# Kernel optimization log

Hardware: AMD Instinct MI355X
Metric: run time of the kernel (lower is better)

Reference implementation:

```python
import jax, jax.numpy as jnp
import numpy as np
import math

NEG_INF = -10000.0

def setup_inputs() -> dict:
    key = jax.random.key(0)
    k1, k2, k3 = jax.random.split(key, 3)
    B, Sq, Sk, H, D = 2, 2048, 2048, 16, 64
    q = jax.random.normal(k1, (B, Sq, H, D), dtype=jnp.float32)
    kv = jax.random.normal(k2, (B, Sk, 2, H, D), dtype=jnp.float32)
    key_padding_mask = jax.random.randint(k3, (B, Sk), 0, 2).astype(jnp.bool_)
    return {"q": q, "kv": kv, "key_padding_mask": key_padding_mask}

def reference(q, kv, key_padding_mask):
    # q: (B, Sq, H, D); kv: (B, Sk, 2, H, D); key_padding_mask: (B, Sk) True=keep
    D = q.shape[-1]
    softmax_scale = 1.0 / math.sqrt(D)
    k = kv[:, :, 0]  # (B, Sk, H, D)
    v = kv[:, :, 1]  # (B, Sk, H, D)
    # (B, H, Sq, Sk) score matrix
    scores = jnp.einsum('bthd,bshd->bhts', q, k * softmax_scale)
    # additive padding mask: 0 where keep, NEG_INF where masked out
    pad = jnp.where(key_padding_mask, 0.0, NEG_INF).astype(scores.dtype)
    scores = scores + pad[:, None, None, :]
    attention = jax.nn.softmax(scores, axis=-1)
    # dropout_p = 0.0 (eval mode) -> no-op
    output = jnp.einsum('bhts,bshd->bthd', attention, v)
    return output
```

## Files before the change

### kernel.cpp

```cpp
#include <hip/hip_runtime.h>

typedef unsigned short u16;
typedef unsigned int   u32;
typedef u16   u16x8 __attribute__((ext_vector_type(8)));
typedef float f32x4 __attribute__((ext_vector_type(4)));
typedef float f32x16 __attribute__((ext_vector_type(16)));
typedef __bf16 bf16x8 __attribute__((ext_vector_type(8)));
typedef u32   u32x4 __attribute__((ext_vector_type(4)));

#define QSCALE  0.18033688011112f
#define BM_OPEN  -28.8539008177793f
#define BM_MASK  -14455.8043097f

__device__ __forceinline__ u16 f2bf(float x){
  __bf16 h = (__bf16)x;
  return __builtin_bit_cast(u16, h);
}
__device__ __forceinline__ f32x16 mfma32(u16x8 a, u16x8 b, f32x16 c){
  return __builtin_amdgcn_mfma_f32_32x32x16_bf16(
      __builtin_bit_cast(bf16x8, a), __builtin_bit_cast(bf16x8, b), c, 0, 0, 0);
}
__device__ __forceinline__ void gld16(const void* g, void* l){
  __builtin_amdgcn_global_load_lds(
      (const __attribute__((address_space(1))) u32*)g,
      (__attribute__((address_space(3))) u32*)l, 16, 0, 0);
}
__device__ __forceinline__ u32 cvtpk(float lo, float hi){
  u32 d;
  asm("v_cvt_pk_bf16_f32 %0, %1, %2" : "=v"(d) : "v"(lo), "v"(hi));
  return d;
}
__device__ __forceinline__ void plswap(u32 &x, u32 &y){
  asm("v_permlane32_swap_b32 %0, %1" : "+v"(x), "+v"(y));
}


__global__ __launch_bounds__(256, 4)
void prepass(const float* __restrict__ KV, const int* __restrict__ MASK,
             u16* __restrict__ IMG, float* __restrict__ BIASM)
{
  const int tid = threadIdx.x;
  const int bid = blockIdx.x;
  const int kt = bid & 31;
  const int h  = (bid >> 5) & 15;
  const int b  = bid >> 9;
  const int kb = kt*64;
  const size_t kv_b = (size_t)b*(2048u*2048u);
  u16* tile = IMG + (size_t)bid * 8192;

  {
    const int skey = tid >> 2, scp = tid & 3;
    const float* kp = KV + kv_b + (size_t)(kb + skey)*2048 + h*64 + 16*scp;
    f32x4 f0 = *(const f32x4*)(kp);
    f32x4 f1 = *(const f32x4*)(kp + 4);
    f32x4 f2 = *(const f32x4*)(kp + 8);
    f32x4 f3 = *(const f32x4*)(kp + 12);
    u16x8 c0, c1;
    #pragma unroll
    for (int e = 0; e < 4; ++e){
      c0[e] = f2bf(f0[e]); c0[e+4] = f2bf(f1[e]);
      c1[e] = f2bf(f2[e]); c1[e+4] = f2bf(f3[e]);
    }
    const int idx0 = skey*64 + (((2*scp) ^ (skey & 7)) << 3);
    *(u16x8*)&tile[idx0]     = c0;
    *(u16x8*)&tile[idx0 ^ 8] = c1;
  }
  {
    const int sdb = tid & 7, ssp = tid >> 3;
    const float* vp = KV + kv_b + (size_t)(kb + 2*ssp)*2048 + 1024 + h*64 + 8*sdb;
    f32x4 r0a = *(const f32x4*)(vp);
    f32x4 r0b = *(const f32x4*)(vp + 4);
    f32x4 r1a = *(const f32x4*)(vp + 2048);
    f32x4 r1b = *(const f32x4*)(vp + 2048 + 4);
    u32* vimg = (u32*)(tile + 4096);
    const int wc = ssp >> 2, wi = ssp & 3;
    #pragma unroll
    for (int j = 0; j < 4; ++j){
      const int d0 = 8*sdb + j;
      const int d1 = d0 + 4;
      vimg[d0*32 + ((wc ^ (d0 & 7)) << 2) + wi] = (u32)f2bf(r0a[j]) | ((u32)f2bf(r1a[j]) << 16);
      vimg[d1*32 + ((wc ^ (d1 & 7)) << 2) + wi] = (u32)f2bf(r0b[j]) | ((u32)f2bf(r1b[j]) << 16);
    }
  }
  if (h == 0 && tid < 64){
    const int s = kb + tid;
    BIASM[b*2048 + s] = MASK[b*2048 + s] ? BM_OPEN : BM_MASK;
  }
}

template<int PRE>
__global__ __launch_bounds__(256, 2)
void attn_main(const float* __restrict__ Q, const float* __restrict__ KV,
               const int* __restrict__ MASK, const u16* __restrict__ IMG,
               const float* __restrict__ BIASM, float* __restrict__ OUT)
{
  __shared__ __align__(16) u16 KVbuf[3][8192];
  __shared__ __align__(16) float BiasLds[2048];

  const int tid  = threadIdx.x;
  const int w    = tid >> 6;
  const int lane = tid & 63;
  const int hi   = lane >> 5;
  const int lq   = lane & 31;

  const int bid0 = blockIdx.x;
  const int bid  = (bid0 & 7)*64 + (bid0 >> 3);
  const int qt  = bid & 15;
  const int h   = (bid >> 4) & 15;
  const int b   = bid >> 8;

  const int qbase = qt*128 + w*32;
  const size_t q_b  = (size_t)b * (2048u*1024u);
  const size_t kv_b = (size_t)b * (2048u*2048u);

  const int sw7 = lq & 7;

  u16x8 Qf[4];
  {
    const int qrow = qbase + lq;
    const float* qp = Q + q_b + (size_t)qrow*1024 + h*64 + 8*hi;
    #pragma unroll
    for (int kc = 0; kc < 4; ++kc){
      f32x4 a = *(const f32x4*)(qp + 16*kc);
      f32x4 c = *(const f32x4*)(qp + 16*kc + 4);
      u16x8 v;
      #pragma unroll
      for (int e = 0; e < 4; ++e){
        v[e]     = f2bf(a[e] * QSCALE);
        v[e + 4] = f2bf(c[e] * QSCALE);
      }
      Qf[kc] = v;
    }
  }

  f32x16 Oa[2];
  #pragma unroll
  for (int dt = 0; dt < 2; ++dt)
    #pragma unroll
    for (int r = 0; r < 16; ++r) Oa[dt][r] = 0.f;
  float lrun = 0.f;

  const char* img0 = (const char*)IMG + (size_t)((b*16 + h)*32) * 16384;
  const int so = tid*16;
  const int skey = tid >> 2, scp = tid & 3;
  const int sdb  = tid & 7,  ssp = tid >> 3;
  const float* kp0 = KV + kv_b + (size_t)skey*2048 + h*64 + 16*scp;
  const float* vp0 = KV + kv_b + (size_t)(2*ssp)*2048 + 1024 + h*64 + 8*sdb;
  f32x4 kf0, kf1, kf2, kf3, va, vb2, vc, vd;

#define STAGE_ISSUE(T, DST) do{                                               \
    const char* g_ = img0 + (size_t)(T)*16384;                                \
    char* l_ = (char*)(DST);                                                  \
    gld16(g_+so,        l_+so);                                               \
    gld16(g_+so+4096,   l_+so+4096);                                          \
    gld16(g_+so+8192,   l_+so+8192);                                          \
    gld16(g_+so+12288,  l_+so+12288);                                         \
  }while(0)

#define BIAS_STAGE() do{                                                      \
    const char* gb_ = (const char*)BIASM + (size_t)b*8192;                    \
    char* lb_ = (char*)BiasLds;                                               \
    gld16(gb_+so,      lb_+so);                                               \
    gld16(gb_+so+4096, lb_+so+4096);                                          \
  }while(0)

#define STAGE_REG(T) do{                                                      \
    const float* kp_ = kp0 + (size_t)(T)*64*2048;                             \
    kf0=*(const f32x4*)(kp_);   kf1=*(const f32x4*)(kp_+4);                   \
    kf2=*(const f32x4*)(kp_+8); kf3=*(const f32x4*)(kp_+12);                  \
    const float* vp_ = vp0 + (size_t)(T)*64*2048;                             \
    va=*(const f32x4*)(vp_);      vb2=*(const f32x4*)(vp_+4);                 \
    vc=*(const f32x4*)(vp_+2048); vd =*(const f32x4*)(vp_+2048+4);            \
  }while(0)

#define STAGE_WRITE(DST) do{                                                  \
    u16x8 c0_, c1_;                                                           \
    _Pragma("unroll") for (int e_=0; e_<4; ++e_){                             \
      c0_[e_]=f2bf(kf0[e_]); c0_[e_+4]=f2bf(kf1[e_]);                         \
      c1_[e_]=f2bf(kf2[e_]); c1_[e_+4]=f2bf(kf3[e_]); }                       \
    const int kix_ = skey*64 + (((2*scp) ^ (skey & 7)) << 3);                 \
    *(u16x8*)&(DST)[kix_]     = c0_;                                          \
    *(u16x8*)&(DST)[kix_ ^ 8] = c1_;                                          \
    u32* vimg_ = (u32*)((DST)+4096);                                          \
    const int wc_ = ssp >> 2, wi_ = ssp & 3;                                  \
    _Pragma("unroll") for (int j_=0; j_<4; ++j_){                             \
      const int d0_=8*sdb+j_, d1_=d0_+4;                                      \
      vimg_[d0_*32 + ((wc_ ^ (d0_&7)) << 2) + wi_] = (u32)f2bf(va[j_])  | ((u32)f2bf(vc[j_])<<16); \
      vimg_[d1_*32 + ((wc_ ^ (d1_&7)) << 2) + wi_] = (u32)f2bf(vb2[j_]) | ((u32)f2bf(vd[j_])<<16); \
    }                                                                         \
  }while(0)

#define COMPUTE(T, CUR) do{                                                   \
    const u16* Kb_ = (CUR);                                                   \
    const u32* vimg_ = (const u32*)((CUR) + 4096);                            \
    f32x16 S[2];                                                              \
    _Pragma("unroll") for (int ct = 0; ct < 2; ++ct){                         \
      _Pragma("unroll") for (int m = 0; m < 4; ++m){                          \
        f32x4 bq;                                                             \
        if constexpr (PRE){                                                   \
          bq = *(const f32x4*)&BiasLds[(T)*64 + 32*ct + 8*m + 4*hi];          \
        } else {                                                              \
          const int4 mv = *(const int4*)(MASK + b*2048 + (T)*64 + 32*ct + 8*m + 4*hi); \
          bq[0] = mv.x ? BM_OPEN : BM_MASK;                                   \
          bq[1] = mv.y ? BM_OPEN : BM_MASK;                                   \
          bq[2] = mv.z ? BM_OPEN : BM_MASK;                                   \
          bq[3] = mv.w ? BM_OPEN : BM_MASK;                                   \
        }                                                                     \
        S[ct][4*m+0] = bq[0]; S[ct][4*m+1] = bq[1];                           \
        S[ct][4*m+2] = bq[2]; S[ct][4*m+3] = bq[3];                           \
      }                                                                       \
    }                                                                         \
    __builtin_amdgcn_s_setprio(1);                                            \
    _Pragma("unroll") for (int ct = 0; ct < 2; ++ct){                         \
      _Pragma("unroll") for (int kc = 0; kc < 4; ++kc){                       \
        u16x8 kf = *(const u16x8*)&Kb_[(32*ct + lq)*64 + (((2*kc + hi) ^ sw7) << 3)]; \
        S[ct] = mfma32(kf, Qf[kc], S[ct]);                                    \
      }                                                                       \
    }                                                                         \
    __builtin_amdgcn_s_setprio(0);                                            \
    u32 pa[2][4], pb[2][4];                                                   \
    float ps = 0.f;                                                           \
    _Pragma("unroll") for (int ct = 0; ct < 2; ++ct){                         \
      _Pragma("unroll") for (int m = 0; m < 4; ++m){                          \
        const float p0 = __builtin_amdgcn_exp2f(S[ct][4*m+0]);                \
        const float p1 = __builtin_amdgcn_exp2f(S[ct][4*m+1]);                \
        const float p2 = __builtin_amdgcn_exp2f(S[ct][4*m+2]);                \
        const float p3 = __builtin_amdgcn_exp2f(S[ct][4*m+3]);                \
        ps += (p0 + p1) + (p2 + p3);                                          \
        pa[ct][m] = cvtpk(p0, p1);                                            \
        pb[ct][m] = cvtpk(p2, p3);                                            \
      }                                                                       \
    }                                                                         \
    lrun += ps;                                                               \
               \
    u16x8 Pf[4];                                                              \
    _Pragma("unroll") for (int ct = 0; ct < 2; ++ct){                         \
      plswap(pa[ct][0], pa[ct][1]);  plswap(pb[ct][0], pb[ct][1]);            \
      plswap(pa[ct][2], pa[ct][3]);  plswap(pb[ct][2], pb[ct][3]);            \
      u32x4 f0_ = { pa[ct][0], pb[ct][0], pa[ct][1], pb[ct][1] };             \
      u32x4 f1_ = { pa[ct][2], pb[ct][2], pa[ct][3], pb[ct][3] };             \
      Pf[2*ct+0] = __builtin_bit_cast(u16x8, f0_);                            \
      Pf[2*ct+1] = __builtin_bit_cast(u16x8, f1_);                            \
    }                                                                         \
    __builtin_amdgcn_s_setprio(1);                                            \
    _Pragma("unroll") for (int dt = 0; dt < 2; ++dt){                         \
      _Pragma("unroll") for (int sc = 0; sc < 4; ++sc){                       \
        u32x4 vv = *(const u32x4*)&vimg_[(32*dt + lq)*32 + (((2*sc + hi) ^ sw7) << 2)]; \
        Oa[dt] = mfma32(__builtin_bit_cast(u16x8, vv), Pf[sc], Oa[dt]);       \
      }                                                                       \
    }                                                                         \
    __builtin_amdgcn_s_setprio(0);                                            \
  }while(0)

#define SEAM(N) do{                                                           \
    __builtin_amdgcn_sched_barrier(0);                                        \
    asm volatile("s_waitcnt vmcnt(%0)" :: "i"(N) : "memory");                 \
    __builtin_amdgcn_sched_barrier(0);                                        \
    __builtin_amdgcn_s_barrier();                                             \
  }while(0)

#define PITER(T, CUR, FREE) do{                                               \
    if ((T) + 2 <= 31) STAGE_ISSUE((T)+2, FREE);                              \
    COMPUTE(T, CUR);                                                          \
    SEAM(4);                                                                  \
  }while(0)

  if constexpr (PRE){
    u16* b0 = &KVbuf[0][0];
    u16* b1 = &KVbuf[1][0];
    u16* b2 = &KVbuf[2][0];
    BIAS_STAGE();
    STAGE_ISSUE(0, b0);
    STAGE_ISSUE(1, b1);
    SEAM(4);
    for (int u = 0; u < 10; ++u){
      PITER(3*u    , b0, b2);
      PITER(3*u + 1, b1, b0);
      PITER(3*u + 2, b2, b1);
    }
    COMPUTE(30, b0);
    SEAM(0);
    COMPUTE(31, b1);
  } else {
    STAGE_REG(0);
    STAGE_WRITE(&KVbuf[0][0]);
    __syncthreads();
    for (int t = 0; t < 32; ++t){
      if (t < 31) STAGE_REG(t+1);
      COMPUTE(t, &KVbuf[t & 1][0]);
      if (t < 31){
        STAGE_WRITE(&KVbuf[(t+1) & 1][0]);
        __syncthreads();
      }
    }
  }

  {
    float l_ = lrun + __shfl_xor(lrun, 32, 64);
    const float inv = 1.f / l_;
    const int qrow = qbase + lq;
    float* op = OUT + q_b + (size_t)qrow*1024 + h*64;
    #pragma unroll
    for (int dt = 0; dt < 2; ++dt){
      #pragma unroll
      for (int m = 0; m < 4; ++m){
        f32x4 ov;
        ov[0] = Oa[dt][4*m+0] * inv;
        ov[1] = Oa[dt][4*m+1] * inv;
        ov[2] = Oa[dt][4*m+2] * inv;
        ov[3] = Oa[dt][4*m+3] * inv;
        *(f32x4*)(op + 32*dt + 8*m + 4*hi) = ov;
      }
    }
  }
#undef STAGE_ISSUE
#undef BIAS_STAGE
#undef STAGE_REG
#undef STAGE_WRITE
#undef COMPUTE
#undef SEAM
#undef PITER
}

extern "C" void kernel_launch(void* const* d_in, const int* in_sizes, int n_in,
                              void* d_out, int out_size, void* d_ws, size_t ws_size,
                              hipStream_t stream)
{
  const float* Q  = nullptr;
  const float* KV = nullptr;
  const int*   M  = nullptr;
  for (int i = 0; i < n_in; ++i){
    if      (in_sizes[i] == 4194304) Q  = (const float*)d_in[i];
    else if (in_sizes[i] == 8388608) KV = (const float*)d_in[i];
    else if (in_sizes[i] == 4096)    M  = (const int*)d_in[i];
  }
  if (!Q)  Q  = (const float*)d_in[0];
  if (!KV) KV = (const float*)d_in[1];
  if (!M)  M  = (const int*)d_in[2];
  float* O = (float*)d_out;

  const size_t NEED = 16384ull + 1024ull*16384ull;
  if (ws_size >= NEED){
    float* biasm = (float*)d_ws;
    u16*   img   = (u16*)((char*)d_ws + 16384);
    prepass<<<dim3(1024), dim3(256), 0, stream>>>(KV, M, img, biasm);
    attn_main<1><<<dim3(512), dim3(256), 0, stream>>>(Q, KV, M, img, biasm, O);
  } else {
    attn_main<0><<<dim3(512), dim3(256), 0, stream>>>(Q, KV, M, nullptr, nullptr, O);
  }
}
```

Before: 59.91 us.

## Shrink KV staging to double buffer and raise occupancy to three blocks per CU

Drops the triple-buffered LDS ring with explicit vmcnt waits and unrolled 3-way pipeline. It uses a plain double-buffered loop with __syncthreads, and raises launch bounds from 2 to 3 blocks per CU. Less LDS per block plus the tighter register cap should let more blocks share a CU and hide latency through occupancy. The cost is a shallower prefetch: the __syncthreads after each tile likely waits on outstanding global_load_lds traffic. The tighter register budget may also cause spills.

```diff
diff --git a/kernel.cpp b/kernel.cpp
--- a/kernel.cpp
+++ b/kernel.cpp
@@ -89,16 +89,15 @@
 }
 
 template<int PRE>
-__global__ __launch_bounds__(256, 2)
+__global__ __launch_bounds__(256, 3)
 void attn_main(const float* __restrict__ Q, const float* __restrict__ KV,
                const int* __restrict__ MASK, const u16* __restrict__ IMG,
                const float* __restrict__ BIASM, float* __restrict__ OUT)
 {
-  __shared__ __align__(16) u16 KVbuf[3][8192];
+  __shared__ __align__(16) u16 KVbuf[2][8192];
   __shared__ __align__(16) float BiasLds[2048];
 
   const int tid  = threadIdx.x;
-  const int w    = tid >> 6;
   const int lane = tid & 63;
   const int hi   = lane >> 5;
   const int lq   = lane & 31;
@@ -109,6 +108,7 @@
   const int h   = (bid >> 4) & 15;
   const int b   = bid >> 8;
 
+  const int w    = tid >> 6;
   const int qbase = qt*128 + w*32;
   const size_t q_b  = (size_t)b * (2048u*1024u);
   const size_t kv_b = (size_t)b * (2048u*2048u);
@@ -213,7 +213,7 @@
     __builtin_amdgcn_s_setprio(1);                                            \
     _Pragma("unroll") for (int ct = 0; ct < 2; ++ct){                         \
       _Pragma("unroll") for (int kc = 0; kc < 4; ++kc){                       \
-        u16x8 kf = *(const u16x8*)&Kb_[(32*ct + lq)*64 + (((2*kc + hi) ^ sw7) << 3)]; \
+        u16x8 kf = *(const u16x8*)&Kb_[(32*ct + lq)*64 + (((2*kc+hi)^sw7)<<3)]; \
         S[ct] = mfma32(kf, Qf[kc], S[ct]);                                    \
       }                                                                       \
     }                                                                         \
@@ -232,7 +232,6 @@
       }                                                                       \
     }                                                                         \
     lrun += ps;                                                               \
-               \
     u16x8 Pf[4];                                                              \
     _Pragma("unroll") for (int ct = 0; ct < 2; ++ct){                         \
       plswap(pa[ct][0], pa[ct][1]);  plswap(pb[ct][0], pb[ct][1]);            \
@@ -245,53 +244,31 @@
     __builtin_amdgcn_s_setprio(1);                                            \
     _Pragma("unroll") for (int dt = 0; dt < 2; ++dt){                         \
       _Pragma("unroll") for (int sc = 0; sc < 4; ++sc){                       \
-        u32x4 vv = *(const u32x4*)&vimg_[(32*dt + lq)*32 + (((2*sc + hi) ^ sw7) << 2)]; \
+        u32x4 vv = *(const u32x4*)&vimg_[(32*dt + lq)*32 + (((2*sc+hi)^sw7)<<2)]; \
         Oa[dt] = mfma32(__builtin_bit_cast(u16x8, vv), Pf[sc], Oa[dt]);       \
       }                                                                       \
     }                                                                         \
     __builtin_amdgcn_s_setprio(0);                                            \
   }while(0)
 
-#define SEAM(N) do{                                                           \
-    __builtin_amdgcn_sched_barrier(0);                                        \
-    asm volatile("s_waitcnt vmcnt(%0)" :: "i"(N) : "memory");                 \
-    __builtin_amdgcn_sched_barrier(0);                                        \
-    __builtin_amdgcn_s_barrier();                                             \
-  }while(0)
-
-#define PITER(T, CUR, FREE) do{                                               \
-    if ((T) + 2 <= 31) STAGE_ISSUE((T)+2, FREE);                              \
-    COMPUTE(T, CUR);                                                          \
-    SEAM(4);                                                                  \
-  }while(0)
-
   if constexpr (PRE){
-    u16* b0 = &KVbuf[0][0];
-    u16* b1 = &KVbuf[1][0];
-    u16* b2 = &KVbuf[2][0];
     BIAS_STAGE();
-    STAGE_ISSUE(0, b0);
-    STAGE_ISSUE(1, b1);
-    SEAM(4);
-    for (int u = 0; u < 10; ++u){
-      PITER(3*u    , b0, b2);
-      PITER(3*u + 1, b1, b0);
-      PITER(3*u + 2, b2, b1);
-    }
-    COMPUTE(30, b0);
-    SEAM(0);
-    COMPUTE(31, b1);
+    STAGE_ISSUE(0, &KVbuf[0][0]);
   } else {
     STAGE_REG(0);
     STAGE_WRITE(&KVbuf[0][0]);
-    __syncthreads();
-    for (int t = 0; t < 32; ++t){
-      if (t < 31) STAGE_REG(t+1);
-      COMPUTE(t, &KVbuf[t & 1][0]);
-      if (t < 31){
-        STAGE_WRITE(&KVbuf[(t+1) & 1][0]);
-        __syncthreads();
-      }
+  }
+  __syncthreads();
+
+  for (int t = 0; t < 32; ++t){
+    if (t < 31){
+      if constexpr (PRE) STAGE_ISSUE(t+1, &KVbuf[(t+1) & 1][0]);
+      else               STAGE_REG(t+1);
+    }
+    COMPUTE(t, &KVbuf[t & 1][0]);
+    if (t < 31){
+      if constexpr (!PRE) STAGE_WRITE(&KVbuf[(t+1) & 1][0]);
+      __syncthreads();
     }
   }
 
@@ -318,8 +295,6 @@
 #undef STAGE_REG
 #undef STAGE_WRITE
 #undef COMPUTE
-#undef SEAM
-#undef PITER
 }
 
 extern "C" void kernel_launch(void* const* d_in, const int* in_sizes, int n_in,
```

New measurement: 62.80 us. 4.8% more time.
